# Kernel tuning notes

Measured on AMD Instinct MI355X. Metric: run time of the kernel, lower is better.

The kernel has to match this reference:

```python
import jax, jax.numpy as jnp
import numpy as np
from jax import lax

B, C, H, W = 8, 2, 1024, 1024
K = 500            # max_num
POST_MAX = 83      # circle_nms post_max_size
NMS_THRESH = 4.0   # squared-distance threshold in grid units
SCORE_THR = 0.1
# post_center_range converted to grid units per CenterPointBBoxCoder.__init__
PCR_LOW = jnp.array([-100.0, -100.0, -10.0], dtype=jnp.float32)
PCR_HIGH = jnp.array([1124.0, 1124.0, 10.0], dtype=jnp.float32)


def setup_inputs() -> dict:
    key = jax.random.key(0)
    ks = jax.random.split(key, 7)
    return {
        "heat": jax.random.uniform(ks[0], (B, C, H, W), dtype=jnp.float32),
        "reg": jax.random.normal(ks[1], (B, 2, H, W), dtype=jnp.float32),
        "rot_sine": jax.random.normal(ks[2], (B, 1, H, W), dtype=jnp.float32),
        "rot_cosine": jax.random.normal(ks[3], (B, 1, H, W), dtype=jnp.float32),
        "hei": jax.random.normal(ks[4], (B, 1, H, W), dtype=jnp.float32),
        "dim": jax.random.normal(ks[5], (B, 3, H, W), dtype=jnp.float32),
        "vel": jax.random.normal(ks[6], (B, 2, H, W), dtype=jnp.float32),
    }


def _gather_feat(feat_bnc, inds_bk):
    # feat: [B, N, Ch], inds: [B, K] -> [B, K, Ch]
    return jnp.take_along_axis(feat_bnc, inds_bk[:, :, None], axis=1)


def _transpose_and_gather(feat_bchw, inds_bk):
    # [B, Ch, H, W] -> gather at flat HW indices -> [B, K, Ch]
    b, c, h, w = feat_bchw.shape
    f = feat_bchw.transpose(0, 2, 3, 1).reshape(b, h * w, c)
    return _gather_feat(f, inds_bk)


def _topk(scores):
    # scores: [B, C, H, W]
    b, c, h, w = scores.shape
    topk_scores, topk_inds = lax.top_k(scores.reshape(b, c, h * w), K)  # [B,C,K]
    topk_inds = topk_inds % (h * w)
    topk_ys = (topk_inds // w).astype(jnp.float32)
    topk_xs = (topk_inds % w).astype(jnp.float32)
    topk_score, topk_ind = lax.top_k(topk_scores.reshape(b, c * K), K)  # [B,K]
    topk_clses = (topk_ind // K).astype(jnp.int32)
    gather2 = lambda t: jnp.take_along_axis(t.reshape(b, c * K), topk_ind, axis=1)
    return topk_score, gather2(topk_inds), topk_clses, gather2(topk_ys), gather2(topk_xs)


def _circle_nms_keep(x, y, s):
    # Sequential circle NMS per image (jit-compatible fori_loop).
    k = x.shape[0]
    order = jnp.argsort(-s)
    xs, ys = x[order], y[order]
    idx = jnp.arange(k)

    def body(i, supp):
        d2 = (xs - xs[i]) ** 2 + (ys - ys[i]) ** 2
        new = supp | ((idx > i) & (d2 <= NMS_THRESH))
        return jnp.where(supp[i], supp, new)

    supp = lax.fori_loop(0, k, body, jnp.zeros(k, dtype=bool))
    keep_sorted = ~supp
    keep_sorted = keep_sorted & (jnp.cumsum(keep_sorted.astype(jnp.int32)) <= POST_MAX)
    return jnp.zeros(k, dtype=bool).at[order].set(keep_sorted)


def reference(heat, reg, rot_sine, rot_cosine, hei, dim, vel):
    scores, inds, clses, ys, xs = _topk(heat)            # [B,K] each
    reg_g = _transpose_and_gather(reg, inds)             # [B,K,2]
    xs = xs[:, :, None] + reg_g[:, :, 0:1]
    ys = ys[:, :, None] + reg_g[:, :, 1:2]
    rot = jnp.arctan2(_transpose_and_gather(rot_sine, inds),
                      _transpose_and_gather(rot_cosine, inds))  # [B,K,1]
    hei_g = _transpose_and_gather(hei, inds)             # [B,K,1]
    dim_g = _transpose_and_gather(dim, inds)             # [B,K,3]
    vel_g = _transpose_and_gather(vel, inds)             # [B,K,2]
    boxes = jnp.concatenate([xs, ys, hei_g, dim_g, rot, vel_g], axis=2)  # [B,K,9]

    valid = (boxes[..., :3] >= PCR_LOW).all(-1) & (boxes[..., :3] <= PCR_HIGH).all(-1)
    valid = valid & (scores > SCORE_THR)

    nms_scores = jnp.where(valid, scores, -1e9)
    keep = jax.vmap(_circle_nms_keep)(boxes[..., 0], boxes[..., 1], nms_scores) & valid
    return boxes, scores, clses.astype(jnp.float32), valid, keep
```

## Files before the change

### kernel.cpp

```cpp
#include <hip/hip_runtime.h>
#include <stdint.h>

typedef unsigned int u32;
typedef unsigned long long u64;

#define HW (1024*1024)
#define KTOP 500
#define CAP 8192u
#define LCAP 256u
#define POST_MAX 83
#define DELTA_THR 9728u

#define WS_CNT   0
#define WS_CAND  32768
#define WS_SORT  1081344
#define WS_XY    1146880
#define WS_ORDV  1179648
#define WS_NV    1196032


__global__ __launch_bounds__(256) void k1_collect(const float* __restrict__ heat,
                                                  u32* cnt, uint2* cand){
  __shared__ uint2 lbuf[LCAP];
  __shared__ u32 lcnt, gbase;
  int s     = blockIdx.x >> 7;
  int chunk = blockIdx.x & 127;
  int tid   = threadIdx.x;
  if (tid == 0) lcnt = 0;
  __syncthreads();
  const float4* hp = (const float4*)(heat + (size_t)s*HW + (size_t)chunk*8192);
  float4 v[8];
  #pragma unroll
  for (int i = 0; i < 8; ++i) v[i] = hp[i*256 + tid];
  #pragma unroll
  for (int i = 0; i < 8; ++i){
    u32 idx0 = (u32)chunk*8192u + (u32)(i*256 + tid)*4u;
    float vals[4] = {v[i].x, v[i].y, v[i].z, v[i].w};
    #pragma unroll
    for (int c = 0; c < 4; ++c){
      u32 bits  = __float_as_uint(vals[c]);
      u32 delta = 0x3F800000u - bits;
      if (delta < DELTA_THR){
        u32 p = atomicAdd(&lcnt, 1u);
        if (p < LCAP) lbuf[p] = make_uint2(bits, idx0 + (u32)c);
        else {
          u32 gp = atomicAdd(&cnt[s*16], 1u);
          if (gp < CAP) cand[(size_t)s*CAP + gp] = make_uint2(bits, idx0 + (u32)c);
        }
      }
    }
  }
  __syncthreads();
  u32 n = (lcnt < LCAP) ? lcnt : LCAP;
  if (tid == 0) gbase = atomicAdd(&cnt[s*16], n);
  __syncthreads();
  for (u32 i = tid; i < n; i += 256){
    u32 p = gbase + i;
    if (p < CAP) cand[(size_t)s*CAP + p] = lbuf[i];
  }
}

__global__ __launch_bounds__(1024) void kR_rank(const float* __restrict__ heat,
                                                const u32* __restrict__ cnt,
                                                uint2* cand, uint2* sorted){
  __shared__ __align__(16) u64 lkey[CAP];
  __shared__ u32 lhist[256];
  __shared__ u32 lc;
  __shared__ int t2s;
  int s = blockIdx.x >> 1, h = blockIdx.x & 1, t = threadIdx.x;
  u32 n = cnt[s*16]; if (n > CAP) n = CAP;

  if (n < (u32)KTOP){
    if (h) return;
    if (t < 256) lhist[t] = 0;
    if (t == 0) lc = 0;
    __syncthreads();
    const float4* hp = (const float4*)(heat + (size_t)s*HW);
    for (int it = 0; it < 256; ++it){
      float4 v = hp[it*1024 + t];
      #pragma unroll
      for (int c = 0; c < 4; ++c){
        float val = (c==0)?v.x:(c==1)?v.y:(c==2)?v.z:v.w;
        u32 bits  = __float_as_uint(val);
        u32 delta = 0x3F800000u - bits;
        u32 bin   = delta >> 16; if (bin > 255u) bin = 255u;
        atomicAdd(&lhist[bin], 1u);
      }
    }
    __syncthreads();
    if (t == 0){
      u32 cum = 0; u32 b1 = 255u;
      for (u32 bb = 0; bb < 256u; ++bb){
        cum += lhist[bb];
        if (cum >= (u32)KTOP){ b1 = bb; break; }
      }
      t2s = (int)(0x3F800000u - ((b1 + 1u) << 16) + 1u);
    }
    __syncthreads();
    int t2 = t2s;
    for (int it = 0; it < 256; ++it){
      float4 v = hp[it*1024 + t];
      u32 idx0 = (u32)(it*1024 + t)*4u;
      #pragma unroll
      for (int c = 0; c < 4; ++c){
        float val = (c==0)?v.x:(c==1)?v.y:(c==2)?v.z:v.w;
        int bits = (int)__float_as_uint(val);
        if (bits >= t2){
          u32 p = atomicAdd(&lc, 1u);
          if (p < CAP) cand[(size_t)s*CAP + p] = make_uint2((u32)bits, idx0 + (u32)c);
        }
      }
    }
    __syncthreads();
    n = (lc < CAP) ? lc : CAP;
  }

  for (u32 i = t; i < n; i += 1024){
    uint2 cv = cand[(size_t)s*CAP + i];
    lkey[i] = ((u64)(~cv.x) << 32) | (u64)cv.y;
  }
  __syncthreads();

  u32 lo = (n < (u32)KTOP) ? 0u : (u32)h * ((n + 1u) >> 1);
  u32 hi = (n < (u32)KTOP) ? n : ((h ? n : ((n + 1u) >> 1)));
  const ulonglong2* lk2 = (const ulonglong2*)lkey;
  for (u32 me = lo + t; me < hi; me += 1024){
    u64 k0 = lkey[me];
    u32 r = 0;
    u32 half = n >> 1;
    for (u32 j = 0; j < half; ++j){
      ulonglong2 kk = lk2[j];
      r += (kk.x < k0) ? 1u : 0u;
      r += (kk.y < k0) ? 1u : 0u;
    }
    if (n & 1u) r += (lkey[n-1] < k0) ? 1u : 0u;
    if (r < 512u)
      sorted[s*512 + (int)r] = make_uint2(~(u32)(k0 >> 32), (u32)k0);
  }
}

__global__ __launch_bounds__(1024) void kT1_prep(const uint2* __restrict__ sorted,
                                                 const float* __restrict__ reg,
                                                 const float* __restrict__ rots,
                                                 const float* __restrict__ rotc,
                                                 const float* __restrict__ hei,
                                                 const float* __restrict__ dim,
                                                 const float* __restrict__ vel,
                                                 float* out, float2* xyg,
                                                 u32* ordvg, u32* nvg){
  __shared__ u64 k2a[512], k2b[512];
  __shared__ uint2 fin[512];
  __shared__ float xo[512], yo[512];
  __shared__ int order[512], vld[512];
  __shared__ int wsum[16];
  int b = blockIdx.x, t = threadIdx.x;

  uint2 mye = make_uint2(0u, 0u);
  if (t < 512){
    mye = sorted[(b*2 + 0)*512 + t];
    k2a[t] = ((u64)(~mye.x) << 32) | (u64)t;
  } else {
    int p = t - 512;
    mye = sorted[(b*2 + 1)*512 + p];
    k2b[p] = ((u64)(~mye.x) << 32) | (u64)(KTOP + p);
  }
  __syncthreads();

  if (t < KTOP){
    u64 K = k2a[t];
    int lo = 0, hi = KTOP;
    while (lo < hi){ int mid = (lo + hi) >> 1; if (k2b[mid] < K) lo = mid + 1; else hi = mid; }
    int m = t + lo;
    if (m < KTOP){
      fin[m] = make_uint2(mye.x, mye.y & 0xFFFFFu);
      out[36000 + b*KTOP + m] = __uint_as_float(mye.x);
      out[40000 + b*KTOP + m] = 0.0f;
    }
  } else if (t >= 512 && t < 512 + KTOP){
    int p = t - 512;
    u64 K = k2b[p];
    int lo = 0, hi = KTOP;
    while (lo < hi){ int mid = (lo + hi) >> 1; if (k2a[mid] < K) lo = mid + 1; else hi = mid; }
    int m = p + lo;
    if (m < KTOP){
      fin[m] = make_uint2(mye.x, (mye.y & 0xFFFFFu) | (1u << 20));
      out[36000 + b*KTOP + m] = __uint_as_float(mye.x);
      out[40000 + b*KTOP + m] = 1.0f;
    }
  }
  __syncthreads();

  float x = 0.f, y = 0.f; int v = 0;
  if (t < KTOP){
    uint2 e = fin[t];
    u32 ind = e.y & 0xFFFFFu;
    float mysc = __uint_as_float(e.x);
    float xs0 = (float)(ind & 1023u);
    float ys0 = (float)(ind >> 10);
    size_t bb = (size_t)b;
    float r0  = reg [(bb*2 + 0)*HW + ind];
    float r1  = reg [(bb*2 + 1)*HW + ind];
    float sn  = rots[ bb       *HW + ind];
    float cs  = rotc[ bb       *HW + ind];
    float he  = hei [ bb       *HW + ind];
    float d0  = dim [(bb*3 + 0)*HW + ind];
    float d1  = dim [(bb*3 + 1)*HW + ind];
    float d2v = dim [(bb*3 + 2)*HW + ind];
    float v0  = vel [(bb*2 + 0)*HW + ind];
    float v1  = vel [(bb*2 + 1)*HW + ind];
    x = xs0 + r0; y = ys0 + r1;
    float rot = atan2f(sn, cs);
    float* bx = out + (size_t)(b*KTOP + t)*9;
    bx[0]=x; bx[1]=y; bx[2]=he; bx[3]=d0; bx[4]=d1; bx[5]=d2v; bx[6]=rot; bx[7]=v0; bx[8]=v1;
    v = ((x >= -100.0f) && (x <= 1124.0f) &&
         (y >= -100.0f) && (y <= 1124.0f) &&
         (he >= -10.0f) && (he <= 10.0f) && (mysc > 0.1f)) ? 1 : 0;
    out[44000 + b*KTOP + t] = v ? 1.0f : 0.0f;
  }
  if (t < 512){ xo[t] = x; yo[t] = y; vld[t] = v; }

  u64 bm = __ballot(v != 0);
  int lane = t & 63, wv = t >> 6;
  if (lane == 0) wsum[wv] = __popcll(bm);
  __syncthreads();
  int off = 0, nValid = 0;
  #pragma unroll
  for (int w2 = 0; w2 < 8; ++w2){
    int sv = wsum[w2];
    nValid += sv;
    if (w2 < wv) off += sv;
  }
  int incl = off + __popcll(bm & ((~0ull) >> (63 - lane)));
  if (t < KTOP){
    int excl = incl - v;
    int slot = v ? excl : (nValid + (t - excl));
    order[slot] = t;
  }
  __syncthreads();

  if (t < KTOP){
    int p = order[t];
    xyg[b*512 + t] = make_float2(xo[p], yo[p]);
    ordvg[b*512 + t] = (u32)p | ((u32)vld[p] << 31);
  } else if (t < 512){
    xyg[b*512 + t] = make_float2(1e30f, 1e30f);
    ordvg[b*512 + t] = 0u;
  }
  if (t == 0) nvg[b] = (u32)nValid;
}

__global__ __launch_bounds__(64) void kT2_greedy(const float2* __restrict__ xyg,
                                                 const u32* __restrict__ ordvg,
                                                 const u32* __restrict__ nvg,
                                                 float* out){
  __shared__ float2 pts[512];
  __shared__ u64 keepw[8];
  int b = blockIdx.x, t = threadIdx.x;
  const float2* src = xyg + b*512;
  for (int i = t; i < 512; i += 64) pts[i] = src[i];
  if (t < 8) keepw[t] = 0ull;
  __syncthreads();
  int nv = (int)nvg[b];

  float kx0 = 1e30f, ky0 = 1e30f, kx1 = 1e30f, ky1 = 1e30f;
  int count = 0;
  u64 curw = 0ull;
  int i = 0;
  float2 pcur = pts[0];
  float2 pnxt = pts[1];
  for (i = 0; i < nv; ++i){
    float2 p = pcur;
    pcur = pnxt;
    pnxt = pts[(i + 2 < 512) ? (i + 2) : 511];
    float dx0 = __fsub_rn(kx0, p.x), dy0 = __fsub_rn(ky0, p.y);
    float dx1 = __fsub_rn(kx1, p.x), dy1 = __fsub_rn(ky1, p.y);
    float d20 = __fadd_rn(__fmul_rn(dx0,dx0), __fmul_rn(dy0,dy0));
    float d21 = __fadd_rn(__fmul_rn(dx1,dx1), __fmul_rn(dy1,dy1));
    bool nearby = (d20 <= 4.0f) || (d21 <= 4.0f);
    if (!__any(nearby)){
      curw |= (1ull << (i & 63));
      if (count < 64){
        if (t == count){ kx0 = p.x; ky0 = p.y; }
      } else {
        if (t == count - 64){ kx1 = p.x; ky1 = p.y; }
      }
      ++count;
      if (count == POST_MAX) break;
    }
    if ((i & 63) == 63){
      if (t == 0) keepw[i >> 6] |= curw;
      curw = 0ull;
    }
  }
  if (t == 0 && curw != 0ull){
    int wi = i >> 6; if (wi > 7) wi = 7;
    keepw[wi] |= curw;
  }
  __syncthreads();

  for (int e = t; e < KTOP; e += 64){
    int bit = (int)((keepw[e >> 6] >> (e & 63)) & 1ull);
    u32 pv = ordvg[b*512 + e];
    int p = (int)(pv & 511u);
    out[48000 + b*KTOP + p] = (bit && (pv >> 31)) ? 1.0f : 0.0f;
  }
}

extern "C" void kernel_launch(void* const* d_in, const int* in_sizes, int n_in,
                              void* d_out, int out_size, void* d_ws, size_t ws_size,
                              hipStream_t stream){
  const float* heat = (const float*)d_in[0];
  const float* reg  = (const float*)d_in[1];
  const float* rots = (const float*)d_in[2];
  const float* rotc = (const float*)d_in[3];
  const float* hei  = (const float*)d_in[4];
  const float* dim  = (const float*)d_in[5];
  const float* vel  = (const float*)d_in[6];
  float* out = (float*)d_out;
  char* ws = (char*)d_ws;
  u32*    cnt    = (u32*)   (ws + WS_CNT);
  uint2*  cand   = (uint2*) (ws + WS_CAND);
  uint2*  sorted = (uint2*) (ws + WS_SORT);
  float2* xyg    = (float2*)(ws + WS_XY);
  u32*    ordvg  = (u32*)   (ws + WS_ORDV);
  u32*    nvg    = (u32*)   (ws + WS_NV);

  (void)hipMemsetAsync(ws, 0, 1024, stream);
  k1_collect <<<2048, 256, 0, stream>>>(heat, cnt, cand);
  kR_rank    <<<32,  1024, 0, stream>>>(heat, cnt, cand, sorted);
  kT1_prep   <<<8,   1024, 0, stream>>>(sorted, reg, rots, rotc, hei, dim, vel, out, xyg, ordvg, nvg);
  kT2_greedy <<<8,     64, 0, stream>>>(xyg, ordvg, nvg, out);
}
```

Before: 61.88 us.

## Use per-chunk candidate slots, drop memset, fuse prep and greedy NMS kernels

Candidate collection now writes each block's candidates to a fixed 64-slot region with a per-chunk count word, replacing global atomics and removing the workspace memset. The rank kernel prefix-sums the 128 chunk counts and compacts candidates into shared memory, falling back to a full histogram rescan if any chunk overflows. The prep and greedy circle-NMS kernels are fused into one kernel that passes points through shared memory instead of global memory, which removes one launch and a global round trip. In exchange, one thread serially scans 128 counts, and the fused kernel leaves most of its 1024 threads idle during the 64-thread greedy loop.

```diff
diff --git a/kernel.cpp b/kernel.cpp
--- a/kernel.cpp
+++ b/kernel.cpp
@@ -7,22 +7,18 @@
 #define HW (1024*1024)
 #define KTOP 500
 #define CAP 8192u
-#define LCAP 256u
 #define POST_MAX 83
 #define DELTA_THR 9728u
 
-#define WS_CNT   0
+#define WS_CNT2  0
 #define WS_CAND  32768
 #define WS_SORT  1081344
-#define WS_XY    1146880
-#define WS_ORDV  1179648
-#define WS_NV    1196032
 
 
 __global__ __launch_bounds__(256) void k1_collect(const float* __restrict__ heat,
-                                                  u32* cnt, uint2* cand){
-  __shared__ uint2 lbuf[LCAP];
-  __shared__ u32 lcnt, gbase;
+                                                  u32* cnt2, uint2* cand){
+  __shared__ uint2 lbuf[64];
+  __shared__ u32 lcnt;
   int s     = blockIdx.x >> 7;
   int chunk = blockIdx.x & 127;
   int tid   = threadIdx.x;
@@ -42,35 +38,56 @@
       u32 delta = 0x3F800000u - bits;
       if (delta < DELTA_THR){
         u32 p = atomicAdd(&lcnt, 1u);
-        if (p < LCAP) lbuf[p] = make_uint2(bits, idx0 + (u32)c);
-        else {
-          u32 gp = atomicAdd(&cnt[s*16], 1u);
-          if (gp < CAP) cand[(size_t)s*CAP + gp] = make_uint2(bits, idx0 + (u32)c);
-        }
-      }
-    }
-  }
-  __syncthreads();
-  u32 n = (lcnt < LCAP) ? lcnt : LCAP;
-  if (tid == 0) gbase = atomicAdd(&cnt[s*16], n);
-  __syncthreads();
-  for (u32 i = tid; i < n; i += 256){
-    u32 p = gbase + i;
-    if (p < CAP) cand[(size_t)s*CAP + p] = lbuf[i];
-  }
+        if (p < 64u) lbuf[p] = make_uint2(bits, idx0 + (u32)c);
+      }
+    }
+  }
+  __syncthreads();
+  u32 n = lcnt;
+  u32 stored = (n < 64u) ? n : 64u;
+  if (tid < stored) cand[(size_t)s*CAP + (u32)chunk*64u + tid] = lbuf[tid];
+  if (tid == 0) cnt2[s*128 + chunk] = stored | ((n > 64u) ? 0x80000000u : 0u);
 }
 
 __global__ __launch_bounds__(1024) void kR_rank(const float* __restrict__ heat,
-                                                const u32* __restrict__ cnt,
+                                                const u32* __restrict__ cnt2,
                                                 uint2* cand, uint2* sorted){
   __shared__ __align__(16) u64 lkey[CAP];
+  __shared__ u32 coff[129];
   __shared__ u32 lhist[256];
   __shared__ u32 lc;
   __shared__ int t2s;
+  __shared__ u32 meta;
   int s = blockIdx.x >> 1, h = blockIdx.x & 1, t = threadIdx.x;
-  u32 n = cnt[s*16]; if (n > CAP) n = CAP;
-
-  if (n < (u32)KTOP){
+
+  if (t == 0){
+    u32 tot = 0, ov = 0;
+    for (int c = 0; c < 128; ++c){
+      u32 w = cnt2[s*128 + c];
+      ov |= (w >> 31);
+      coff[c] = tot;
+      tot += (w & 0x7FFFFFFFu);
+    }
+    coff[128] = tot;
+    meta = tot | (ov << 31);
+  }
+  __syncthreads();
+  u32 total = meta & 0x7FFFFFFFu;
+  bool fb = ((meta >> 31) != 0u) || (total < (u32)KTOP);
+  u32 n;
+
+  if (!fb){
+    n = total;
+    for (u32 i = t; i < CAP; i += 1024){
+      u32 c = i >> 6, j = i & 63u;
+      u32 cnt_c = coff[c+1] - coff[c];
+      if (j < cnt_c){
+        uint2 cv = cand[(size_t)s*CAP + i];
+        lkey[coff[c] + j] = ((u64)(~cv.x) << 32) | (u64)cv.y;
+      }
+    }
+    __syncthreads();
+  } else {
     if (h) return;
     if (t < 256) lhist[t] = 0;
     if (t == 0) lc = 0;
@@ -113,16 +130,15 @@
     }
     __syncthreads();
     n = (lc < CAP) ? lc : CAP;
-  }
-
-  for (u32 i = t; i < n; i += 1024){
-    uint2 cv = cand[(size_t)s*CAP + i];
-    lkey[i] = ((u64)(~cv.x) << 32) | (u64)cv.y;
-  }
-  __syncthreads();
-
-  u32 lo = (n < (u32)KTOP) ? 0u : (u32)h * ((n + 1u) >> 1);
-  u32 hi = (n < (u32)KTOP) ? n : ((h ? n : ((n + 1u) >> 1)));
+    for (u32 i = t; i < n; i += 1024){
+      uint2 cv = cand[(size_t)s*CAP + i];
+      lkey[i] = ((u64)(~cv.x) << 32) | (u64)cv.y;
+    }
+    __syncthreads();
+  }
+
+  u32 lo = fb ? 0u : (u32)h * ((n + 1u) >> 1);
+  u32 hi = fb ? n  : (h ? n : ((n + 1u) >> 1));
   const ulonglong2* lk2 = (const ulonglong2*)lkey;
   for (u32 me = lo + t; me < hi; me += 1024){
     u64 k0 = lkey[me];
@@ -139,20 +155,22 @@
   }
 }
 
-__global__ __launch_bounds__(1024) void kT1_prep(const uint2* __restrict__ sorted,
-                                                 const float* __restrict__ reg,
-                                                 const float* __restrict__ rots,
-                                                 const float* __restrict__ rotc,
-                                                 const float* __restrict__ hei,
-                                                 const float* __restrict__ dim,
-                                                 const float* __restrict__ vel,
-                                                 float* out, float2* xyg,
-                                                 u32* ordvg, u32* nvg){
+__global__ __launch_bounds__(1024) void kT_tail(const uint2* __restrict__ sorted,
+                                                const float* __restrict__ reg,
+                                                const float* __restrict__ rots,
+                                                const float* __restrict__ rotc,
+                                                const float* __restrict__ hei,
+                                                const float* __restrict__ dim,
+                                                const float* __restrict__ vel,
+                                                float* out){
   __shared__ u64 k2a[512], k2b[512];
   __shared__ uint2 fin[512];
   __shared__ float xo[512], yo[512];
+  __shared__ float2 pts[512];
   __shared__ int order[512], vld[512];
+  __shared__ u32 ordvl[512];
   __shared__ int wsum[16];
+  __shared__ u64 keepw[8];
   int b = blockIdx.x, t = threadIdx.x;
 
   uint2 mye = make_uint2(0u, 0u);
@@ -164,6 +182,7 @@
     mye = sorted[(b*2 + 1)*512 + p];
     k2b[p] = ((u64)(~mye.x) << 32) | (u64)(KTOP + p);
   }
+  if (t < 8) keepw[t] = 0ull;
   __syncthreads();
 
   if (t < KTOP){
@@ -240,67 +259,56 @@
 
   if (t < KTOP){
     int p = order[t];
-    xyg[b*512 + t] = make_float2(xo[p], yo[p]);
-    ordvg[b*512 + t] = (u32)p | ((u32)vld[p] << 31);
+    pts[t] = make_float2(xo[p], yo[p]);
+    ordvl[t] = (u32)p | ((u32)vld[p] << 31);
   } else if (t < 512){
-    xyg[b*512 + t] = make_float2(1e30f, 1e30f);
-    ordvg[b*512 + t] = 0u;
-  }
-  if (t == 0) nvg[b] = (u32)nValid;
-}
-
-__global__ __launch_bounds__(64) void kT2_greedy(const float2* __restrict__ xyg,
-                                                 const u32* __restrict__ ordvg,
-                                                 const u32* __restrict__ nvg,
-                                                 float* out){
-  __shared__ float2 pts[512];
-  __shared__ u64 keepw[8];
-  int b = blockIdx.x, t = threadIdx.x;
-  const float2* src = xyg + b*512;
-  for (int i = t; i < 512; i += 64) pts[i] = src[i];
-  if (t < 8) keepw[t] = 0ull;
-  __syncthreads();
-  int nv = (int)nvg[b];
-
-  float kx0 = 1e30f, ky0 = 1e30f, kx1 = 1e30f, ky1 = 1e30f;
-  int count = 0;
-  u64 curw = 0ull;
-  int i = 0;
-  float2 pcur = pts[0];
-  float2 pnxt = pts[1];
-  for (i = 0; i < nv; ++i){
-    float2 p = pcur;
-    pcur = pnxt;
-    pnxt = pts[(i + 2 < 512) ? (i + 2) : 511];
-    float dx0 = __fsub_rn(kx0, p.x), dy0 = __fsub_rn(ky0, p.y);
-    float dx1 = __fsub_rn(kx1, p.x), dy1 = __fsub_rn(ky1, p.y);
-    float d20 = __fadd_rn(__fmul_rn(dx0,dx0), __fmul_rn(dy0,dy0));
-    float d21 = __fadd_rn(__fmul_rn(dx1,dx1), __fmul_rn(dy1,dy1));
-    bool nearby = (d20 <= 4.0f) || (d21 <= 4.0f);
-    if (!__any(nearby)){
-      curw |= (1ull << (i & 63));
-      if (count < 64){
-        if (t == count){ kx0 = p.x; ky0 = p.y; }
-      } else {
-        if (t == count - 64){ kx1 = p.x; ky1 = p.y; }
-      }
-      ++count;
-      if (count == POST_MAX) break;
-    }
-    if ((i & 63) == 63){
-      if (t == 0) keepw[i >> 6] |= curw;
-      curw = 0ull;
-    }
-  }
-  if (t == 0 && curw != 0ull){
-    int wi = i >> 6; if (wi > 7) wi = 7;
-    keepw[wi] |= curw;
-  }
-  __syncthreads();
-
-  for (int e = t; e < KTOP; e += 64){
-    int bit = (int)((keepw[e >> 6] >> (e & 63)) & 1ull);
-    u32 pv = ordvg[b*512 + e];
+    pts[t] = make_float2(1e30f, 1e30f);
+    ordvl[t] = 0u;
+  }
+  __syncthreads();
+
+  if (t < 64){
+    int nv = nValid;
+    float kx0 = 1e30f, ky0 = 1e30f, kx1 = 1e30f, ky1 = 1e30f;
+    int count = 0;
+    u64 curw = 0ull;
+    int i = 0;
+    float2 pcur = pts[0];
+    float2 pnxt = pts[1];
+    for (i = 0; i < nv; ++i){
+      float2 p = pcur;
+      pcur = pnxt;
+      pnxt = pts[(i + 2 < 512) ? (i + 2) : 511];
+      float dx0 = __fsub_rn(kx0, p.x), dy0 = __fsub_rn(ky0, p.y);
+      float dx1 = __fsub_rn(kx1, p.x), dy1 = __fsub_rn(ky1, p.y);
+      float d20 = __fadd_rn(__fmul_rn(dx0,dx0), __fmul_rn(dy0,dy0));
+      float d21 = __fadd_rn(__fmul_rn(dx1,dx1), __fmul_rn(dy1,dy1));
+      bool nearby = (d20 <= 4.0f) || (d21 <= 4.0f);
+      if (!__any(nearby)){
+        curw |= (1ull << (i & 63));
+        if (count < 64){
+          if (t == count){ kx0 = p.x; ky0 = p.y; }
+        } else {
+          if (t == count - 64){ kx1 = p.x; ky1 = p.y; }
+        }
+        ++count;
+        if (count == POST_MAX) break;
+      }
+      if ((i & 63) == 63){
+        if (t == 0) keepw[i >> 6] |= curw;
+        curw = 0ull;
+      }
+    }
+    if (t == 0 && curw != 0ull){
+      int wi = i >> 6; if (wi > 7) wi = 7;
+      keepw[wi] |= curw;
+    }
+  }
+  __syncthreads();
+
+  if (t < KTOP){
+    int bit = (int)((keepw[t >> 6] >> (t & 63)) & 1ull);
+    u32 pv = ordvl[t];
     int p = (int)(pv & 511u);
     out[48000 + b*KTOP + p] = (bit && (pv >> 31)) ? 1.0f : 0.0f;
   }
@@ -318,16 +326,11 @@
   const float* vel  = (const float*)d_in[6];
   float* out = (float*)d_out;
   char* ws = (char*)d_ws;
-  u32*    cnt    = (u32*)   (ws + WS_CNT);
-  uint2*  cand   = (uint2*) (ws + WS_CAND);
-  uint2*  sorted = (uint2*) (ws + WS_SORT);
-  float2* xyg    = (float2*)(ws + WS_XY);
-  u32*    ordvg  = (u32*)   (ws + WS_ORDV);
-  u32*    nvg    = (u32*)   (ws + WS_NV);
-
-  (void)hipMemsetAsync(ws, 0, 1024, stream);
-  k1_collect <<<2048, 256, 0, stream>>>(heat, cnt, cand);
-  kR_rank    <<<32,  1024, 0, stream>>>(heat, cnt, cand, sorted);
-  kT1_prep   <<<8,   1024, 0, stream>>>(sorted, reg, rots, rotc, hei, dim, vel, out, xyg, ordvg, nvg);
-  kT2_greedy <<<8,     64, 0, stream>>>(xyg, ordvg, nvg, out);
+  u32*   cnt2   = (u32*)  (ws + WS_CNT2);
+  uint2* cand   = (uint2*)(ws + WS_CAND);
+  uint2* sorted = (uint2*)(ws + WS_SORT);
+
+  k1_collect <<<2048, 256, 0, stream>>>(heat, cnt2, cand);
+  kR_rank    <<<32,  1024, 0, stream>>>(heat, cnt2, cand, sorted);
+  kT_tail    <<<8,   1024, 0, stream>>>(sorted, reg, rots, rotc, hei, dim, vel, out);
 }
```

Result: faster. 54.82 us (-11.4%).
